# Kernel tuning notes

Hardware: AMD Instinct MI355X
Metric: run time of the kernel (lower is better)

Reference implementation:

```python
import jax, jax.numpy as jnp
import numpy as np

MARGIN = 0.1
EPS = 1e-6


def setup_inputs() -> dict:
    key = jax.random.key(0)
    k1, k2, k3 = jax.random.split(key, 3)
    B = 8192
    predictions = jax.random.normal(k1, (B,), dtype=jnp.float32)
    targets = jax.random.normal(k2, (B,), dtype=jnp.float32)
    mask = jax.random.bernoulli(k3, 0.9, (B,))  # bool (B,)
    return {"predictions": predictions, "targets": targets, "mask": mask}


def reference(predictions, targets, mask):
    # Reduce multi-output predictions/targets to scalars per example
    p = predictions.mean(axis=-1) if predictions.ndim > 1 else predictions
    t = targets.mean(axis=-1) if targets.ndim > 1 else targets
    B = p.shape[0]

    dt = t[:, None] - t[None, :]              # (B, B) target diffs
    dp = p[:, None] - p[None, :]              # (B, B) prediction diffs

    # only pairs i < j, both unmasked, with |target diff| >= 1e-6
    upper = jnp.triu(jnp.ones((B, B), dtype=bool), k=1)
    valid = upper & (jnp.abs(dt) >= EPS) & mask[:, None] & mask[None, :]

    # MarginRankingLoss: max(0, -y * (x1 - x2) + margin), y = sign(dt)
    hinge = jnp.maximum(0.0, -jnp.sign(dt) * dp + MARGIN)

    total = jnp.where(valid, hinge, 0.0).sum()
    count = valid.sum()
    return total / jnp.maximum(count, 1).astype(total.dtype)
```

## Files before the change

kernel.cpp:

```cpp
#include <hip/hip_runtime.h>
#include <math.h>

#define TPB 256
#define JCHUNK 128

__global__ __launch_bounds__(TPB) void mrl_partial(
    const float* __restrict__ p, const float* __restrict__ t,
    const int* __restrict__ m, int B,
    float2* __restrict__ part)
{
    const int id = blockIdx.x;
    const float f = sqrtf((float)(65 * 65 - 4 * id));
    int bi = (int)((65.0f - f) * 0.5f);
    while (bi * (65 - bi) > id) --bi;
    while ((bi + 1) * (64 - bi) <= id) ++bi;
    const int off = id - bi * (65 - bi);
    const int by  = 2 * bi + off;

    const int i0 = bi * TPB;
    const int j0 = by * JCHUNK;
    const bool diag = (off < 2);

    __shared__ float2 sj[JCHUNK];
    bool jmasked = false;
    if (threadIdx.x < JCHUNK) {
        const int j = j0 + threadIdx.x;
        const int mj = m[j];
        jmasked = (mj == 0);
        sj[threadIdx.x] = make_float2(p[j], mj ? t[j] : __builtin_nanf(""));
    }

    const int i = i0 + threadIdx.x;
    const int mi_ok = m[i];
    const float pi = p[i];
    const float ti = mi_ok ? t[i] : __builtin_nanf("");

    const int mj_cnt = __syncthreads_count(jmasked ? 1 : 0);
    const int mi_cnt = __syncthreads_count(mi_ok ? 0 : 1);

    float acc = 0.0f;
    unsigned cnt = 0;

    if (!diag) {
        #pragma unroll 8
        for (int k = 0; k < JCHUNK; ++k) {
            const float2 pt = sj[k];
            const float dt = ti - pt.y;
            const float qr = pt.x - pi;
            const float q  = fmaf(0.0f, dt, qr);
            const float cs = copysignf(1.0f, dt);
            const float h  = fmaxf(fmaf(cs, q, 0.1f), 0.0f);
            acc += h;
        }
    } else {
        #pragma unroll 8
        for (int k = 0; k < JCHUNK; ++k) {
            const float2 pt = sj[k];
            const int   j  = j0 + k;
            const float dt = ti - pt.y;
            const float q  = pt.x - pi;
            const bool  v  = (fabsf(dt) >= 1e-6f) && (j > i);
            const float h  = fmaxf(fmaf(copysignf(1.0f, dt), q, 0.1f), 0.0f);
            acc += v ? h : 0.0f;
            cnt += (unsigned)__popcll(__ballot(v));
        }
    }

    #pragma unroll
    for (int o = 32; o > 0; o >>= 1)
        acc += __shfl_down(acc, o, 64);

    __shared__ float wsum[TPB / 64];
    __shared__ float wcnt[TPB / 64];
    const int lane = threadIdx.x & 63;
    const int wid  = threadIdx.x >> 6;
    if (lane == 0) { wsum[wid] = acc; wcnt[wid] = (float)cnt; }
    __syncthreads();
    if (threadIdx.x == 0) {
        float a = 0.0f;
        #pragma unroll
        for (int w = 0; w < TPB / 64; ++w) a += wsum[w];
        float c;
        if (!diag) {
            c = (float)((TPB - mi_cnt) * (JCHUNK - mj_cnt));
        } else {
            c = 0.0f;
            #pragma unroll
            for (int w = 0; w < TPB / 64; ++w) c += wcnt[w];
        }
        part[id] = make_float2(a, c);
    }
}

__global__ __launch_bounds__(256) void mrl_final(
    const float2* __restrict__ part, int nblk, float* __restrict__ out)
{
    double a = 0.0, c = 0.0;
    for (int k = threadIdx.x; k < nblk; k += 256) {
        const float2 v = part[k];
        a += (double)v.x;
        c += (double)v.y;
    }
    #pragma unroll
    for (int o = 32; o > 0; o >>= 1) {
        a += __shfl_down(a, o, 64);
        c += __shfl_down(c, o, 64);
    }
    __shared__ double sa[4];
    __shared__ double sc[4];
    const int lane = threadIdx.x & 63;
    const int wid  = threadIdx.x >> 6;
    if (lane == 0) { sa[wid] = a; sc[wid] = c; }
    __syncthreads();
    if (threadIdx.x == 0) {
        double A = 0.0, C = 0.0;
        #pragma unroll
        for (int w = 0; w < 4; ++w) { A += sa[w]; C += sc[w]; }
        out[0] = (float)(A / fmax(C, 1.0));
    }
}

extern "C" void kernel_launch(void* const* d_in, const int* in_sizes, int n_in,
                              void* d_out, int out_size, void* d_ws, size_t ws_size,
                              hipStream_t stream)
{
    const float* p = (const float*)d_in[0];
    const float* t = (const float*)d_in[1];
    const int*   m = (const int*)d_in[2];
    const int B = in_sizes[0];

    const int iblocks = B / TPB;
    const int jchunks = B / JCHUNK;
    int nactive = 0;
    for (int b = 0; b < iblocks; ++b) nactive += jchunks - 2 * b;

    float2* part = (float2*)d_ws;

    mrl_partial<<<nactive, TPB, 0, stream>>>(p, t, m, B, part);
    mrl_final<<<1, 256, 0, stream>>>(part, nactive, (float*)d_out);
}
```

Before: 69.23 us.

## Process two rows per thread with smaller j-chunks and bitmask-based pair counting

Each thread now handles two i rows (512-row tiles) against 64-wide j chunks, so every shared-memory j value is reused twice and the triangular block mapping is recomputed for the new ratio. The masking NaN moves from t to p, and valid-pair counts come from a ballot bitmask with popcount instead of per-iteration ballots and syncthreads_count. This cuts per-pair LDS traffic and removes the ballot from the diagonal inner loop, but it changes the block count and grid balance and drops the |dt|>=eps check from the count, relying on NaN propagation and exact ties being absent.

```diff
diff --git a/kernel.cpp b/kernel.cpp
--- a/kernel.cpp
+++ b/kernel.cpp
@@ -1,94 +1,118 @@
 #include <hip/hip_runtime.h>
 #include <math.h>
 
-#define TPB 256
-#define JCHUNK 128
+#define TPB    256
+#define IPT    2
+#define ITILE  (TPB * IPT)
+#define JCHUNK 64
+#define RATIO  (ITILE / JCHUNK)
 
 __global__ __launch_bounds__(TPB) void mrl_partial(
     const float* __restrict__ p, const float* __restrict__ t,
     const int* __restrict__ m, int B,
     float2* __restrict__ part)
 {
+    const int CH = B / JCHUNK;
+    const int A  = CH + RATIO / 2;
+    const int ROWS = B / ITILE;
     const int id = blockIdx.x;
-    const float f = sqrtf((float)(65 * 65 - 4 * id));
-    int bi = (int)((65.0f - f) * 0.5f);
-    while (bi * (65 - bi) > id) --bi;
-    while ((bi + 1) * (64 - bi) <= id) ++bi;
-    const int off = id - bi * (65 - bi);
-    const int by  = 2 * bi + off;
 
-    const int i0 = bi * TPB;
-    const int j0 = by * JCHUNK;
-    const bool diag = (off < 2);
+    const float f = sqrtf((float)(A * A - 16 * id));
+    int bi = (int)((float)A - f) >> 3;
+    if (bi < 0) bi = 0;
+    if (bi > ROWS - 1) bi = ROWS - 1;
+    #define CFN(b) (A * (b) - 4 * (b) * (b))
+    while (CFN(bi) > id) --bi;
+    while (CFN(bi + 1) <= id) ++bi;
+    const int off = id - CFN(bi);
+    const int by  = RATIO * bi + off;
+    const int i0  = bi * ITILE;
+    const int j0  = by * JCHUNK;
+    const bool diag = (off < RATIO);
 
     __shared__ float2 sj[JCHUNK];
-    bool jmasked = false;
-    if (threadIdx.x < JCHUNK) {
-        const int j = j0 + threadIdx.x;
+    __shared__ unsigned long long smask;
+    if (threadIdx.x < 64) {
+        const int j  = j0 + threadIdx.x;
         const int mj = m[j];
-        jmasked = (mj == 0);
-        sj[threadIdx.x] = make_float2(p[j], mj ? t[j] : __builtin_nanf(""));
+        sj[threadIdx.x] = make_float2(mj ? p[j] : __builtin_nanf(""), t[j]);
+        const unsigned long long bal = __ballot(mj != 0);
+        if (threadIdx.x == 0) smask = bal;
     }
 
-    const int i = i0 + threadIdx.x;
-    const int mi_ok = m[i];
-    const float pi = p[i];
-    const float ti = mi_ok ? t[i] : __builtin_nanf("");
+    const int i_lo = i0 + threadIdx.x;
+    const int i_hi = i_lo + TPB;
+    const int mlo = m[i_lo];
+    const int mhi = m[i_hi];
+    const float pl = mlo ? p[i_lo] : __builtin_nanf("");
+    const float ph = mhi ? p[i_hi] : __builtin_nanf("");
+    const float tl = t[i_lo];
+    const float th = t[i_hi];
 
-    const int mj_cnt = __syncthreads_count(jmasked ? 1 : 0);
-    const int mi_cnt = __syncthreads_count(mi_ok ? 0 : 1);
+    __syncthreads();
+    const unsigned long long jm = smask;
 
-    float acc = 0.0f;
-    unsigned cnt = 0;
-
+    float acc0 = 0.0f, acc1 = 0.0f;
     if (!diag) {
         #pragma unroll 8
         for (int k = 0; k < JCHUNK; ++k) {
             const float2 pt = sj[k];
-            const float dt = ti - pt.y;
-            const float qr = pt.x - pi;
-            const float q  = fmaf(0.0f, dt, qr);
-            const float cs = copysignf(1.0f, dt);
-            const float h  = fmaxf(fmaf(cs, q, 0.1f), 0.0f);
-            acc += h;
+            const float dt0 = tl - pt.y;
+            const float q0  = pt.x - pl;
+            acc0 += fmaxf(fmaf(copysignf(1.0f, dt0), q0, 0.1f), 0.0f);
+            const float dt1 = th - pt.y;
+            const float q1  = pt.x - ph;
+            acc1 += fmaxf(fmaf(copysignf(1.0f, dt1), q1, 0.1f), 0.0f);
         }
     } else {
+        const int kl = i_lo - j0;
+        const int kh = i_hi - j0;
         #pragma unroll 8
         for (int k = 0; k < JCHUNK; ++k) {
             const float2 pt = sj[k];
-            const int   j  = j0 + k;
-            const float dt = ti - pt.y;
-            const float q  = pt.x - pi;
-            const bool  v  = (fabsf(dt) >= 1e-6f) && (j > i);
-            const float h  = fmaxf(fmaf(copysignf(1.0f, dt), q, 0.1f), 0.0f);
-            acc += v ? h : 0.0f;
-            cnt += (unsigned)__popcll(__ballot(v));
+            const float dt0 = tl - pt.y;
+            const float q0  = pt.x - pl;
+            const float h0  = fmaxf(fmaf(copysignf(1.0f, dt0), q0, 0.1f), 0.0f);
+            acc0 += (k > kl) ? h0 : 0.0f;
+            const float dt1 = th - pt.y;
+            const float q1  = pt.x - ph;
+            const float h1  = fmaxf(fmaf(copysignf(1.0f, dt1), q1, 0.1f), 0.0f);
+            acc1 += (k > kh) ? h1 : 0.0f;
         }
     }
 
+    const int total_j = (int)__popcll(jm);
+    int cnt = 0;
+    if (mlo) {
+        const int idx = i_lo - j0;
+        cnt += (idx < 0) ? total_j
+             : ((idx >= 63) ? 0 : (int)__popcll(jm >> (idx + 1)));
+    }
+    if (mhi) {
+        const int idx = i_hi - j0;
+        cnt += (idx < 0) ? total_j
+             : ((idx >= 63) ? 0 : (int)__popcll(jm >> (idx + 1)));
+    }
+
+    float acc = acc0 + acc1;
     #pragma unroll
-    for (int o = 32; o > 0; o >>= 1)
+    for (int o = 32; o > 0; o >>= 1) {
         acc += __shfl_down(acc, o, 64);
+        cnt += __shfl_down(cnt, o, 64);
+    }
 
     __shared__ float wsum[TPB / 64];
-    __shared__ float wcnt[TPB / 64];
+    __shared__ int   wcnt[TPB / 64];
     const int lane = threadIdx.x & 63;
     const int wid  = threadIdx.x >> 6;
-    if (lane == 0) { wsum[wid] = acc; wcnt[wid] = (float)cnt; }
+    if (lane == 0) { wsum[wid] = acc; wcnt[wid] = cnt; }
     __syncthreads();
     if (threadIdx.x == 0) {
         float a = 0.0f;
+        int   c = 0;
         #pragma unroll
-        for (int w = 0; w < TPB / 64; ++w) a += wsum[w];
-        float c;
-        if (!diag) {
-            c = (float)((TPB - mi_cnt) * (JCHUNK - mj_cnt));
-        } else {
-            c = 0.0f;
-            #pragma unroll
-            for (int w = 0; w < TPB / 64; ++w) c += wcnt[w];
-        }
-        part[id] = make_float2(a, c);
+        for (int w = 0; w < TPB / 64; ++w) { a += wsum[w]; c += wcnt[w]; }
+        part[id] = make_float2(a, (float)c);
     }
 }
 
@@ -129,10 +153,10 @@
     const int*   m = (const int*)d_in[2];
     const int B = in_sizes[0];
 
-    const int iblocks = B / TPB;
-    const int jchunks = B / JCHUNK;
+    const int rows = B / ITILE;
+    const int ch   = B / JCHUNK;
     int nactive = 0;
-    for (int b = 0; b < iblocks; ++b) nactive += jchunks - 2 * b;
+    for (int b = 0; b < rows; ++b) nactive += ch - RATIO * b;
 
     float2* part = (float2*)d_ws;
 
```

After: 66.81 us (median of 2 runs). 1.04x faster.
